# Kernel tuning notes

Measured on AMD Instinct MI355X. Metric: run time of the kernel, lower is better.

Reference implementation:

```python
import jax, jax.numpy as jnp
import numpy as np
import math


def _align_seq_len(e, target_n):
    # e: (B, H, N_enc, hd) -> (B, H, target_n, hd) via bilinear resize on sqrt grid
    B, H, N_enc, D = e.shape
    if N_enc == target_n:
        return e
    h_e = int(math.sqrt(N_enc))
    h_t = int(math.sqrt(target_n))
    img = jnp.transpose(e, (0, 1, 3, 2)).reshape(B, H, D, h_e, h_e)
    img = jax.image.resize(img, (B, H, D, h_t, h_t), method='bilinear')
    return jnp.transpose(img.reshape(B, H, D, target_n), (0, 1, 3, 2))


def setup_inputs() -> dict:
    key = jax.random.key(0)
    ks = jax.random.split(key, 7)
    B, N, D, H = 4, 1024, 1152, 16
    hd = D // H
    N_enc = 1024
    s_in = 1.0 / math.sqrt(D)
    return {
        'x': jax.random.normal(ks[0], (B, N, D), jnp.float32),
        'enc_k': jax.random.normal(ks[1], (B, H, N_enc, hd), jnp.float32),
        'enc_v': jax.random.normal(ks[2], (B, H, N_enc, hd), jnp.float32),
        'qkv_w': jax.random.normal(ks[3], (3 * D, D), jnp.float32) * s_in,
        'qkv_b': jax.random.normal(ks[4], (3 * D,), jnp.float32) * 0.02,
        'proj_w': jax.random.normal(ks[5], (D, D), jnp.float32) * s_in,
        'proj_b': jax.random.normal(ks[6], (D,), jnp.float32) * 0.02,
        'stage': 2,
    }


def reference(x, enc_k, enc_v, qkv_w, qkv_b, proj_w, proj_b, stage):
    B, N, C = x.shape
    H = enc_k.shape[1]
    hd = C // H
    scale = hd ** (-0.5)

    qkv = (x @ qkv_w.T + qkv_b).reshape(B, N, 3, H, hd)
    qkv = jnp.transpose(qkv, (2, 0, 3, 1, 4))  # (3, B, H, N, hd)
    q, k, v = qkv[0], qkv[1], qkv[2]

    distill_loss = jnp.float32(0.0)
    if stage == 1:
        ek = _align_seq_len(enc_k, N)
        ev = _align_seq_len(enc_v, N)
        attn = jax.nn.softmax(jnp.einsum('bhnd,bhmd->bhnm', q * scale, ek), axis=-1)
        x_out = jnp.einsum('bhnm,bhmd->bhnd', attn, ev)
    elif stage == 2:
        ek = _align_seq_len(enc_k, N)
        ev = _align_seq_len(enc_v, N)
        attn_own = jax.nn.softmax(jnp.einsum('bhnd,bhmd->bhnm', q * scale, k), axis=-1)
        x_out = jnp.einsum('bhnm,bhmd->bhnd', attn_own, v)
        qd = jax.lax.stop_gradient(q)
        attn_enc = jax.nn.softmax(jnp.einsum('bhnd,bhmd->bhnm', qd * scale, ek), axis=-1)
        o_star = jax.lax.stop_gradient(jnp.einsum('bhnm,bhmd->bhnd', attn_enc, ev))
        distill_loss = jnp.mean((x_out - o_star) ** 2)
    else:
        attn = jax.nn.softmax(jnp.einsum('bhnd,bhmd->bhnm', q * scale, k), axis=-1)
        x_out = jnp.einsum('bhnm,bhmd->bhnd', attn, v)

    x_out = jnp.transpose(x_out, (0, 2, 1, 3)).reshape(B, N, C)
    out = x_out @ proj_w.T + proj_b
    return out, distill_loss
```

## Files before the change

kernel.cpp:

```cpp
#include <hip/hip_runtime.h>
#include <hip/hip_bf16.h>

#define PB 4
#define PN 1024
#define PC 1152
#define PH 16
#define PHD 72
#define BH 64
#define QKV_COLS 3456
#define OUT_ELEMS ((size_t)PB*PN*PC)
#define K_DIM 1152

#define CHUNK_HALVES 6144
#define HEAD_HALVES (16*CHUNK_HALVES)
#define BUF_HALVES ((size_t)BH*HEAD_HALVES)

typedef _Float16 half8_t __attribute__((ext_vector_type(8)));
typedef _Float16 half4_t __attribute__((ext_vector_type(4)));
typedef float float4v __attribute__((ext_vector_type(4)));

#define QSCALE (0.11785113019775792f * 1.4426950408889634f)

__device__ __forceinline__ void load16_lds(const _Float16* g, _Float16* l) {
    __builtin_amdgcn_global_load_lds(
        (const __attribute__((address_space(1))) void*)g,
        (__attribute__((address_space(3))) void*)l, 16, 0, 0);
}

__global__ __launch_bounds__(256) void f32_to_f16(
    const float* __restrict__ in, _Float16* __restrict__ out, int n8)
{
    int i = blockIdx.x * 256 + threadIdx.x;
    if (i >= n8) return;
    float4 a = ((const float4*)in)[2 * i];
    float4 b = ((const float4*)in)[2 * i + 1];
    half8_t h;
    h[0] = (_Float16)a.x; h[1] = (_Float16)a.y; h[2] = (_Float16)a.z; h[3] = (_Float16)a.w;
    h[4] = (_Float16)b.x; h[5] = (_Float16)b.y; h[6] = (_Float16)b.z; h[7] = (_Float16)b.w;
    ((half8_t*)out)[i] = h;
}

__global__ __launch_bounds__(256) void zero_qpad(_Float16* __restrict__ qh)
{
    int i = blockIdx.x * 256 + threadIdx.x;
    int chunk = i / 192, within = i - chunk * 192;
    half8_t z = {};
    *(half8_t*)(qh + (size_t)chunk * CHUNK_HALVES + 4608 + within * 8) = z;
}

__global__ __launch_bounds__(256) void enc_convert(
    const float* __restrict__ ek, const float* __restrict__ ev,
    _Float16* __restrict__ ekh, _Float16* __restrict__ evth)
{
    const int bh = blockIdx.y, nblk = blockIdx.x, t = threadIdx.x;
    const float* ksrc = ek + ((size_t)bh * PN + nblk * 64) * PHD;
    const float* vsrc = ev + ((size_t)bh * PN + nblk * 64) * PHD;
    _Float16* kdst = ekh  + ((size_t)bh * 16 + nblk) * CHUNK_HALVES;
    _Float16* vdst = evth + ((size_t)bh * 16 + nblk) * CHUNK_HALVES;
    for (int i = t; i < 64 * 18; i += 256) {
        int n = i / 18, d4 = (i % 18) * 4;
        float4 kv = *(const float4*)&ksrc[n * PHD + d4];
        float4 vv = *(const float4*)&vsrc[n * PHD + d4];
        float ka[4] = {kv.x, kv.y, kv.z, kv.w};
        float va[4] = {vv.x, vv.y, vv.z, vv.w};
#pragma unroll
        for (int kk = 0; kk < 4; ++kk) {
            int d = d4 + kk;
            kdst[(d >> 3) * 512 + n * 8 + (d & 7)] = (_Float16)ka[kk];
            vdst[(n >> 3) * 768 + d * 8 + (n & 7)] = (_Float16)va[kk];
        }
    }
}

template<int MODE>
__global__ __launch_bounds__(256) void gemm_mfma(
    const _Float16* __restrict__ A, const _Float16* __restrict__ Bm,
    const float* __restrict__ bias,
    _Float16* __restrict__ qh, _Float16* __restrict__ kh,
    _Float16* __restrict__ vth, float* __restrict__ out, int c_tiles)
{
    const int t    = threadIdx.x;
    const int lane = t & 63;
    const int w    = t >> 6;
    const int wm   = w >> 1, wn = w & 1;
    const int lrow = lane & 15, quad = lane >> 4;

    const int per_group = c_tiles * 8;
    const int g  = blockIdx.x / per_group;
    const int r_ = blockIdx.x - g * per_group;
    const int m0 = (g * 8 + (r_ & 7)) * 128;
    const int c0 = (r_ >> 3) * 128;

    const bool tr = (MODE == 1) || (c0 < 2 * PC);

    __shared__ _Float16 As[8192];
    __shared__ _Float16 Bs[8192];

    int rowS[4], koff[4], ldsOff[4];
#pragma unroll
    for (int i = 0; i < 4; ++i) {
        int idx = w * 256 + i * 64 + lane;
        int kt2 = idx >> 9, qq = (idx >> 7) & 3;
        rowS[i]   = idx & 127;
        koff[i]   = kt2 * 32 + qq * 8;
        ldsOff[i] = idx * 8;
    }

    const _Float16* aBase = A  + (size_t)m0 * K_DIM;
    const _Float16* bBase = Bm + (size_t)c0 * K_DIM;

    float4v acc[4][4];
#pragma unroll
    for (int ti = 0; ti < 4; ++ti)
#pragma unroll
        for (int tj = 0; tj < 4; ++tj)
            acc[ti][tj] = (float4v){0.f, 0.f, 0.f, 0.f};

    for (int kb = 0; kb < K_DIM; kb += 64) {
        __syncthreads();
#pragma unroll
        for (int i = 0; i < 4; ++i) {
            load16_lds(aBase + (size_t)rowS[i] * K_DIM + kb + koff[i], &As[ldsOff[i]]);
            load16_lds(bBase + (size_t)rowS[i] * K_DIM + kb + koff[i], &Bs[ldsOff[i]]);
        }
        __syncthreads();
#pragma unroll
        for (int s = 0; s < 2; ++s) {
            half8_t af[4], bf[4];
#pragma unroll
            for (int ti = 0; ti < 4; ++ti)
                af[ti] = *(const half8_t*)&As[(((s * 4 + quad) * 128) + wm * 64 + ti * 16 + lrow) * 8];
#pragma unroll
            for (int tj = 0; tj < 4; ++tj)
                bf[tj] = *(const half8_t*)&Bs[(((s * 4 + quad) * 128) + wn * 64 + tj * 16 + lrow) * 8];
            if (tr) {
#pragma unroll
                for (int ti = 0; ti < 4; ++ti)
#pragma unroll
                    for (int tj = 0; tj < 4; ++tj)
                        acc[ti][tj] = __builtin_amdgcn_mfma_f32_16x16x32_f16(
                            bf[tj], af[ti], acc[ti][tj], 0, 0, 0);
            } else {
#pragma unroll
                for (int ti = 0; ti < 4; ++ti)
#pragma unroll
                    for (int tj = 0; tj < 4; ++tj)
                        acc[ti][tj] = __builtin_amdgcn_mfma_f32_16x16x32_f16(
                            af[ti], bf[tj], acc[ti][tj], 0, 0, 0);
            }
        }
    }

    if (MODE == 1) {
#pragma unroll
        for (int tj = 0; tj < 4; ++tj) {
            int cg = c0 + wn * 64 + tj * 16 + quad * 4;
            float4v bv = *(const float4v*)&bias[cg];
#pragma unroll
            for (int ti = 0; ti < 4; ++ti) {
                int m = m0 + wm * 64 + ti * 16 + lrow;
                float4v o;
#pragma unroll
                for (int r = 0; r < 4; ++r) o[r] = acc[ti][tj][r] + bv[r];
                *(float4v*)&out[(size_t)m * PC + cg] = o;
            }
        }
    } else if (tr) {
        const int jq = c0 / PC;
        const float mulv = (jq == 0) ? QSCALE : 1.f;
        _Float16* dstp = (jq == 0) ? qh : kh;
#pragma unroll
        for (int tj = 0; tj < 4; ++tj) {
            int cg  = c0 + wn * 64 + tj * 16 + quad * 4;
            int rem = cg - jq * PC;
            int h   = rem / PHD;
            int ds  = rem - h * PHD;
            float4v bv = *(const float4v*)&bias[cg];
#pragma unroll
            for (int ti = 0; ti < 4; ++ti) {
                int m = m0 + wm * 64 + ti * 16 + lrow;
                int b = m >> 10, n = m & 1023;
                size_t chunk = ((size_t)(b * PH + h) * 16 + (n >> 6)) * CHUNK_HALVES;
                half4_t hv;
#pragma unroll
                for (int r = 0; r < 4; ++r)
                    hv[r] = (_Float16)((acc[ti][tj][r] + bv[r]) * mulv);
                *(half4_t*)&dstp[chunk + (ds >> 3) * 512 + (n & 63) * 8 + (ds & 7)] = hv;
            }
        }
    } else {
#pragma unroll
        for (int tj = 0; tj < 4; ++tj) {
            int c   = c0 + wn * 64 + tj * 16 + lrow;
            int rem = c - 2 * PC;
            int h   = rem / PHD;
            int d   = rem - h * PHD;
            float bv = bias[c];
#pragma unroll
            for (int ti = 0; ti < 4; ++ti) {
                int mg = m0 + wm * 64 + ti * 16 + quad * 4;
                int b = mg >> 10, n = mg & 1023;
                size_t chunk = ((size_t)(b * PH + h) * 16 + (n >> 6)) * CHUNK_HALVES;
                half4_t hv;
#pragma unroll
                for (int r = 0; r < 4; ++r)
                    hv[r] = (_Float16)(acc[ti][tj][r] + bv);
                *(half4_t*)&vth[chunk + ((n & 63) >> 3) * 768 + d * 8 + (n & 7)] = hv;
            }
        }
    }
}

__device__ __forceinline__ void attn_step(
    const half8_t* qf, const _Float16* Ks, const _Float16* Vts, _Float16* Pw,
    float4v* O, float& m_run, float& l_run, int ln, int quad)
{
    float4v accS[4];
#pragma unroll
    for (int ct = 0; ct < 4; ++ct) accS[ct] = (float4v){0.f, 0.f, 0.f, 0.f};
#pragma unroll
    for (int ks = 0; ks < 3; ++ks) {
#pragma unroll
        for (int ct = 0; ct < 4; ++ct) {
            half8_t kf = *(const half8_t*)&Ks[(((ks * 4 + quad) * 64) + ct * 16 + ln) * 8];
            accS[ct] = __builtin_amdgcn_mfma_f32_16x16x32_f16(kf, qf[ks], accS[ct], 0, 0, 0);
        }
    }

    float mx = -1e30f;
#pragma unroll
    for (int ct = 0; ct < 4; ++ct)
#pragma unroll
        for (int r = 0; r < 4; ++r) mx = fmaxf(mx, accS[ct][r]);
    mx = fmaxf(mx, __shfl_xor(mx, 16));
    mx = fmaxf(mx, __shfl_xor(mx, 32));
    float m_new = fmaxf(m_run, mx);
    float alpha = exp2f(m_run - m_new);
    m_run = m_new;

    float lsum = 0.f;
    const int pbase = (quad >> 1) * 128 + ln * 8 + (quad & 1) * 4;
#pragma unroll
    for (int ct = 0; ct < 4; ++ct) {
        half4_t pk;
#pragma unroll
        for (int r = 0; r < 4; ++r) {
            float p = exp2f(accS[ct][r] - m_new);
            lsum += p;
            pk[r] = (_Float16)p;
        }
        *(half4_t*)&Pw[pbase + ct * 256] = pk;
    }
    lsum += __shfl_xor(lsum, 16);
    lsum += __shfl_xor(lsum, 32);
    l_run = l_run * alpha + lsum;

#pragma unroll
    for (int ct = 0; ct < 5; ++ct) O[ct] *= alpha;

#pragma unroll
    for (int ks = 0; ks < 2; ++ks) {
        half8_t pf = *(const half8_t*)&Pw[(ks * 4 + quad) * 128 + ln * 8];
#pragma unroll
        for (int ct = 0; ct < 5; ++ct) {
            half8_t vf = *(const half8_t*)&Vts[(((ks * 4 + quad) * 96) + ct * 16 + ln) * 8];
            O[ct] = __builtin_amdgcn_mfma_f32_16x16x32_f16(vf, pf, O[ct], 0, 0, 0);
        }
    }
}

__global__ __launch_bounds__(256, 4) void attn_fused(
    const _Float16* __restrict__ qh, const _Float16* __restrict__ kh,
    const _Float16* __restrict__ vth,
    const _Float16* __restrict__ ekh, const _Float16* __restrict__ evth,
    _Float16* __restrict__ xouth, float* __restrict__ loss_out)
{
    const int t = threadIdx.x;
    const int lane = t & 63;
    const int w = t >> 6;
    const int ln = lane & 15;
    const int quad = lane >> 4;

    const int lid  = blockIdx.x;
    const int bh   = (lid & 7) * 8 + ((lid >> 3) >> 4);
    const int nblk = (lid >> 3) & 15;

    __shared__ _Float16 Ks[CHUNK_HALVES];
    __shared__ _Float16 Vs[CHUNK_HALVES];
    __shared__ _Float16 Ps[4096];
    __shared__ float red[256];

    _Float16* Pw = Ps + w * 1024;

    const _Float16* qc = qh + ((size_t)bh * 16 + nblk) * CHUNK_HALVES;
    half8_t qf[3];
#pragma unroll
    for (int ks = 0; ks < 3; ++ks)
        qf[ks] = *(const half8_t*)&qc[(((ks * 4 + quad) * 64) + w * 16 + ln) * 8];

    const _Float16* kbo = kh   + (size_t)bh * HEAD_HALVES;
    const _Float16* vbo = vth  + (size_t)bh * HEAD_HALVES;
    const _Float16* kbe = ekh  + (size_t)bh * HEAD_HALVES;
    const _Float16* vbe = evth + (size_t)bh * HEAD_HALVES;

    float4v Oo[5], Oe[5];
#pragma unroll
    for (int ct = 0; ct < 5; ++ct) {
        Oo[ct] = (float4v){0.f, 0.f, 0.f, 0.f};
        Oe[ct] = (float4v){0.f, 0.f, 0.f, 0.f};
    }
    float m_o = -1e30f, l_o = 0.f;
    float m_e = -1e30f, l_e = 0.f;

    for (int kt = 0; kt < 16; ++kt) {
        const _Float16* kc = kbo + (size_t)kt * CHUNK_HALVES;
        const _Float16* vc = vbo + (size_t)kt * CHUNK_HALVES;
        __syncthreads();
#pragma unroll
        for (int i = 0; i < 3; ++i) {
            int u = i * 256 + t;
            load16_lds(kc + u * 8, &Ks[u * 8]);
            load16_lds(vc + u * 8, &Vs[u * 8]);
        }
        __syncthreads();
        attn_step(qf, Ks, Vs, Pw, Oo, m_o, l_o, ln, quad);
    }
    for (int kt = 0; kt < 16; ++kt) {
        const _Float16* kc = kbe + (size_t)kt * CHUNK_HALVES;
        const _Float16* vc = vbe + (size_t)kt * CHUNK_HALVES;
        __syncthreads();
#pragma unroll
        for (int i = 0; i < 3; ++i) {
            int u = i * 256 + t;
            load16_lds(kc + u * 8, &Ks[u * 8]);
            load16_lds(vc + u * 8, &Vs[u * 8]);
        }
        __syncthreads();
        attn_step(qf, Ks, Vs, Pw, Oe, m_e, l_e, ln, quad);
    }

    const float inv_o = 1.0f / l_o;
    const float inv_e = 1.0f / l_e;

    const int b = bh >> 4, h = bh & 15;
    const int nrow = nblk * 64 + w * 16 + ln;

    float lacc = 0.f;
    const size_t rowbase = (size_t)(b * PN + nrow) * PC + h * PHD;
#pragma unroll
    for (int ct = 0; ct < 5; ++ct) {
        int d0 = ct * 16 + quad * 4;
        if (d0 < PHD) {
            half4_t oh;
#pragma unroll
            for (int r = 0; r < 4; ++r) {
                float own = Oo[ct][r] * inv_o;
                oh[r] = (_Float16)own;
                float df = own - Oe[ct][r] * inv_e;
                lacc += df * df;
            }
            *(half4_t*)&xouth[rowbase + d0] = oh;
        }
    }

    red[t] = lacc;
    __syncthreads();
    for (int off = 128; off > 0; off >>= 1) {
        if (t < off) red[t] += red[t + off];
        __syncthreads();
    }
    if (t == 0) atomicAdd(loss_out, red[0] * (1.0f / (float)OUT_ELEMS));
}

extern "C" void kernel_launch(void* const* d_in, const int* in_sizes, int n_in,
                              void* d_out, int out_size, void* d_ws, size_t ws_size,
                              hipStream_t stream)
{
    const float* x      = (const float*)d_in[0];
    const float* enc_k  = (const float*)d_in[1];
    const float* enc_v  = (const float*)d_in[2];
    const float* qkv_w  = (const float*)d_in[3];
    const float* qkv_b  = (const float*)d_in[4];
    const float* proj_w = (const float*)d_in[5];
    const float* proj_b = (const float*)d_in[6];

    float* out = (float*)d_out;

    _Float16* x_h     = (_Float16*)d_ws;
    _Float16* qkvw_h  = x_h + OUT_ELEMS;
    _Float16* projw_h = qkvw_h + (size_t)QKV_COLS * PC;
    _Float16* xout_h  = projw_h + (size_t)PC * PC;
    _Float16* q_h     = xout_h + OUT_ELEMS;
    _Float16* k_h     = q_h  + BUF_HALVES;
    _Float16* vt_h    = k_h  + BUF_HALVES;
    _Float16* ek_h    = vt_h + BUF_HALVES;
    _Float16* evt_h   = ek_h + BUF_HALVES;

    const int n8_x  = (int)(OUT_ELEMS / 8);
    const int n8_qw = QKV_COLS * PC / 8;
    const int n8_pw = PC * PC / 8;

    hipMemsetAsync(out + OUT_ELEMS, 0, sizeof(float), stream);
    zero_qpad<<<768, 256, 0, stream>>>(q_h);

    f32_to_f16<<<(n8_x  + 255) / 256, 256, 0, stream>>>(x,      x_h,     n8_x);
    f32_to_f16<<<(n8_qw + 255) / 256, 256, 0, stream>>>(qkv_w,  qkvw_h,  n8_qw);
    f32_to_f16<<<(n8_pw + 255) / 256, 256, 0, stream>>>(proj_w, projw_h, n8_pw);
    enc_convert<<<dim3(16, BH), 256, 0, stream>>>(enc_k, enc_v, ek_h, evt_h);

    gemm_mfma<0><<<(QKV_COLS / 128) * ((PB * PN) / 128), 256, 0, stream>>>(
        x_h, qkvw_h, qkv_b, q_h, k_h, vt_h, nullptr, QKV_COLS / 128);

    attn_fused<<<16 * BH, 256, 0, stream>>>(
        q_h, k_h, vt_h, ek_h, evt_h, xout_h, out + OUT_ELEMS);

    gemm_mfma<1><<<(PC / 128) * ((PB * PN) / 128), 256, 0, stream>>>(
        xout_h, projw_h, proj_b, nullptr, nullptr, nullptr, out, PC / 128);
}
```

Measured before the change: 342.8 us.

## Merge prep kernels and give each attention wave two query tiles

Five preprocessing launches (three fp32-to-fp16 conversions, Q-pad zeroing, encoder K/V conversion) become one kernel that dispatches on block index, removing launch overhead. The attention kernel now runs 128 threads per block, and each wave handles two 16-row query tiles, so every K/V fragment read from LDS feeds two MFMAs. This halves LDS reads per FLOP and allows more independent MFMAs in flight. The cost is more accumulator registers (four sets of O), fewer waves per block to hide latency, and the removed occupancy hint on launch bounds.

```diff
diff --git a/kernel.cpp b/kernel.cpp
--- a/kernel.cpp
+++ b/kernel.cpp
@@ -27,11 +27,9 @@
         (__attribute__((address_space(3))) void*)l, 16, 0, 0);
 }
 
-__global__ __launch_bounds__(256) void f32_to_f16(
-    const float* __restrict__ in, _Float16* __restrict__ out, int n8)
-{
-    int i = blockIdx.x * 256 + threadIdx.x;
-    if (i >= n8) return;
+__device__ __forceinline__ void cvt8(const float* __restrict__ in,
+                                     _Float16* __restrict__ out, int i)
+{
     float4 a = ((const float4*)in)[2 * i];
     float4 b = ((const float4*)in)[2 * i + 1];
     half8_t h;
@@ -40,34 +38,45 @@
     ((half8_t*)out)[i] = h;
 }
 
-__global__ __launch_bounds__(256) void zero_qpad(_Float16* __restrict__ qh)
-{
-    int i = blockIdx.x * 256 + threadIdx.x;
-    int chunk = i / 192, within = i - chunk * 192;
-    half8_t z = {};
-    *(half8_t*)(qh + (size_t)chunk * CHUNK_HALVES + 4608 + within * 8) = z;
-}
-
-__global__ __launch_bounds__(256) void enc_convert(
+__global__ __launch_bounds__(256) void prep(
+    const float* __restrict__ x, const float* __restrict__ qkv_w,
+    const float* __restrict__ proj_w,
     const float* __restrict__ ek, const float* __restrict__ ev,
+    _Float16* __restrict__ x_h, _Float16* __restrict__ qkvw_h,
+    _Float16* __restrict__ projw_h, _Float16* __restrict__ qh,
     _Float16* __restrict__ ekh, _Float16* __restrict__ evth)
 {
-    const int bh = blockIdx.y, nblk = blockIdx.x, t = threadIdx.x;
-    const float* ksrc = ek + ((size_t)bh * PN + nblk * 64) * PHD;
-    const float* vsrc = ev + ((size_t)bh * PN + nblk * 64) * PHD;
-    _Float16* kdst = ekh  + ((size_t)bh * 16 + nblk) * CHUNK_HALVES;
-    _Float16* vdst = evth + ((size_t)bh * 16 + nblk) * CHUNK_HALVES;
-    for (int i = t; i < 64 * 18; i += 256) {
-        int n = i / 18, d4 = (i % 18) * 4;
-        float4 kv = *(const float4*)&ksrc[n * PHD + d4];
-        float4 vv = *(const float4*)&vsrc[n * PHD + d4];
-        float ka[4] = {kv.x, kv.y, kv.z, kv.w};
-        float va[4] = {vv.x, vv.y, vv.z, vv.w};
-#pragma unroll
-        for (int kk = 0; kk < 4; ++kk) {
-            int d = d4 + kk;
-            kdst[(d >> 3) * 512 + n * 8 + (d & 7)] = (_Float16)ka[kk];
-            vdst[(n >> 3) * 768 + d * 8 + (n & 7)] = (_Float16)va[kk];
+    const int b = blockIdx.x, t = threadIdx.x;
+    if (b < 2304) {
+        cvt8(x, x_h, b * 256 + t);
+    } else if (b < 4248) {
+        cvt8(qkv_w, qkvw_h, (b - 2304) * 256 + t);
+    } else if (b < 4896) {
+        cvt8(proj_w, projw_h, (b - 4248) * 256 + t);
+    } else if (b < 5664) {
+        int i = (b - 4896) * 256 + t;
+        int chunk = i / 192, within = i - chunk * 192;
+        half8_t z = {};
+        *(half8_t*)(qh + (size_t)chunk * CHUNK_HALVES + 4608 + within * 8) = z;
+    } else {
+        int bid = b - 5664;
+        int bh = bid >> 4, nblk = bid & 15;
+        const float* ksrc = ek + ((size_t)bh * PN + nblk * 64) * PHD;
+        const float* vsrc = ev + ((size_t)bh * PN + nblk * 64) * PHD;
+        _Float16* kdst = ekh  + ((size_t)bh * 16 + nblk) * CHUNK_HALVES;
+        _Float16* vdst = evth + ((size_t)bh * 16 + nblk) * CHUNK_HALVES;
+        for (int i = t; i < 64 * 18; i += 256) {
+            int n = i / 18, d4 = (i % 18) * 4;
+            float4 kv = *(const float4*)&ksrc[n * PHD + d4];
+            float4 vv = *(const float4*)&vsrc[n * PHD + d4];
+            float ka[4] = {kv.x, kv.y, kv.z, kv.w};
+            float va[4] = {vv.x, vv.y, vv.z, vv.w};
+#pragma unroll
+            for (int kk = 0; kk < 4; ++kk) {
+                int d = d4 + kk;
+                kdst[(d >> 3) * 512 + n * 8 + (d & 7)] = (_Float16)ka[kk];
+                vdst[(n >> 3) * 768 + d * 8 + (n & 7)] = (_Float16)va[kk];
+            }
         }
     }
 }
@@ -211,65 +220,77 @@
     }
 }
 
-__device__ __forceinline__ void attn_step(
-    const half8_t* qf, const _Float16* Ks, const _Float16* Vts, _Float16* Pw,
-    float4v* O, float& m_run, float& l_run, int ln, int quad)
-{
-    float4v accS[4];
-#pragma unroll
-    for (int ct = 0; ct < 4; ++ct) accS[ct] = (float4v){0.f, 0.f, 0.f, 0.f};
+__device__ __forceinline__ void attn_step2(
+    const half8_t qf[2][3], const _Float16* Ks, const _Float16* Vts,
+    _Float16* P0, _Float16* P1,
+    float4v O0[5], float4v O1[5], float m_run[2], float l_run[2],
+    int ln, int quad)
+{
+    float4v accS[2][4];
+#pragma unroll
+    for (int s = 0; s < 2; ++s)
+#pragma unroll
+        for (int ct = 0; ct < 4; ++ct) accS[s][ct] = (float4v){0.f, 0.f, 0.f, 0.f};
 #pragma unroll
     for (int ks = 0; ks < 3; ++ks) {
 #pragma unroll
         for (int ct = 0; ct < 4; ++ct) {
             half8_t kf = *(const half8_t*)&Ks[(((ks * 4 + quad) * 64) + ct * 16 + ln) * 8];
-            accS[ct] = __builtin_amdgcn_mfma_f32_16x16x32_f16(kf, qf[ks], accS[ct], 0, 0, 0);
-        }
-    }
-
-    float mx = -1e30f;
-#pragma unroll
-    for (int ct = 0; ct < 4; ++ct)
-#pragma unroll
-        for (int r = 0; r < 4; ++r) mx = fmaxf(mx, accS[ct][r]);
-    mx = fmaxf(mx, __shfl_xor(mx, 16));
-    mx = fmaxf(mx, __shfl_xor(mx, 32));
-    float m_new = fmaxf(m_run, mx);
-    float alpha = exp2f(m_run - m_new);
-    m_run = m_new;
-
-    float lsum = 0.f;
+            accS[0][ct] = __builtin_amdgcn_mfma_f32_16x16x32_f16(kf, qf[0][ks], accS[0][ct], 0, 0, 0);
+            accS[1][ct] = __builtin_amdgcn_mfma_f32_16x16x32_f16(kf, qf[1][ks], accS[1][ct], 0, 0, 0);
+        }
+    }
+
     const int pbase = (quad >> 1) * 128 + ln * 8 + (quad & 1) * 4;
 #pragma unroll
-    for (int ct = 0; ct < 4; ++ct) {
-        half4_t pk;
-#pragma unroll
-        for (int r = 0; r < 4; ++r) {
-            float p = exp2f(accS[ct][r] - m_new);
-            lsum += p;
-            pk[r] = (_Float16)p;
-        }
-        *(half4_t*)&Pw[pbase + ct * 256] = pk;
-    }
-    lsum += __shfl_xor(lsum, 16);
-    lsum += __shfl_xor(lsum, 32);
-    l_run = l_run * alpha + lsum;
-
-#pragma unroll
-    for (int ct = 0; ct < 5; ++ct) O[ct] *= alpha;
+    for (int s = 0; s < 2; ++s) {
+        _Float16* Pr = s ? P1 : P0;
+        float mx = -1e30f;
+#pragma unroll
+        for (int ct = 0; ct < 4; ++ct)
+#pragma unroll
+            for (int r = 0; r < 4; ++r) mx = fmaxf(mx, accS[s][ct][r]);
+        mx = fmaxf(mx, __shfl_xor(mx, 16));
+        mx = fmaxf(mx, __shfl_xor(mx, 32));
+        float m_new = fmaxf(m_run[s], mx);
+        float alpha = exp2f(m_run[s] - m_new);
+        m_run[s] = m_new;
+
+        float lsum = 0.f;
+#pragma unroll
+        for (int ct = 0; ct < 4; ++ct) {
+            half4_t pk;
+#pragma unroll
+            for (int r = 0; r < 4; ++r) {
+                float p = exp2f(accS[s][ct][r] - m_new);
+                lsum += p;
+                pk[r] = (_Float16)p;
+            }
+            *(half4_t*)&Pr[pbase + ct * 256] = pk;
+        }
+        lsum += __shfl_xor(lsum, 16);
+        lsum += __shfl_xor(lsum, 32);
+        l_run[s] = l_run[s] * alpha + lsum;
+
+        float4v* O = s ? O1 : O0;
+#pragma unroll
+        for (int ct = 0; ct < 5; ++ct) O[ct] *= alpha;
+    }
 
 #pragma unroll
     for (int ks = 0; ks < 2; ++ks) {
-        half8_t pf = *(const half8_t*)&Pw[(ks * 4 + quad) * 128 + ln * 8];
+        half8_t pf0 = *(const half8_t*)&P0[(ks * 4 + quad) * 128 + ln * 8];
+        half8_t pf1 = *(const half8_t*)&P1[(ks * 4 + quad) * 128 + ln * 8];
 #pragma unroll
         for (int ct = 0; ct < 5; ++ct) {
             half8_t vf = *(const half8_t*)&Vts[(((ks * 4 + quad) * 96) + ct * 16 + ln) * 8];
-            O[ct] = __builtin_amdgcn_mfma_f32_16x16x32_f16(vf, pf, O[ct], 0, 0, 0);
-        }
-    }
-}
-
-__global__ __launch_bounds__(256, 4) void attn_fused(
+            O0[ct] = __builtin_amdgcn_mfma_f32_16x16x32_f16(vf, pf0, O0[ct], 0, 0, 0);
+            O1[ct] = __builtin_amdgcn_mfma_f32_16x16x32_f16(vf, pf1, O1[ct], 0, 0, 0);
+        }
+    }
+}
+
+__global__ __launch_bounds__(128) void attn_fused(
     const _Float16* __restrict__ qh, const _Float16* __restrict__ kh,
     const _Float16* __restrict__ vth,
     const _Float16* __restrict__ ekh, const _Float16* __restrict__ evth,
@@ -288,84 +309,92 @@
     __shared__ _Float16 Ks[CHUNK_HALVES];
     __shared__ _Float16 Vs[CHUNK_HALVES];
     __shared__ _Float16 Ps[4096];
-    __shared__ float red[256];
-
-    _Float16* Pw = Ps + w * 1024;
+    __shared__ float red[128];
+
+    _Float16* P0 = Ps + w * 2048;
+    _Float16* P1 = P0 + 1024;
 
     const _Float16* qc = qh + ((size_t)bh * 16 + nblk) * CHUNK_HALVES;
-    half8_t qf[3];
-#pragma unroll
-    for (int ks = 0; ks < 3; ++ks)
-        qf[ks] = *(const half8_t*)&qc[(((ks * 4 + quad) * 64) + w * 16 + ln) * 8];
+    half8_t qf[2][3];
+#pragma unroll
+    for (int s = 0; s < 2; ++s)
+#pragma unroll
+        for (int ks = 0; ks < 3; ++ks)
+            qf[s][ks] = *(const half8_t*)&qc[(((ks * 4 + quad) * 64) + w * 32 + s * 16 + ln) * 8];
 
     const _Float16* kbo = kh   + (size_t)bh * HEAD_HALVES;
     const _Float16* vbo = vth  + (size_t)bh * HEAD_HALVES;
     const _Float16* kbe = ekh  + (size_t)bh * HEAD_HALVES;
     const _Float16* vbe = evth + (size_t)bh * HEAD_HALVES;
 
-    float4v Oo[5], Oe[5];
+    float4v Oo0[5], Oo1[5], Oe0[5], Oe1[5];
 #pragma unroll
     for (int ct = 0; ct < 5; ++ct) {
-        Oo[ct] = (float4v){0.f, 0.f, 0.f, 0.f};
-        Oe[ct] = (float4v){0.f, 0.f, 0.f, 0.f};
-    }
-    float m_o = -1e30f, l_o = 0.f;
-    float m_e = -1e30f, l_e = 0.f;
+        Oo0[ct] = (float4v){0.f, 0.f, 0.f, 0.f};
+        Oo1[ct] = (float4v){0.f, 0.f, 0.f, 0.f};
+        Oe0[ct] = (float4v){0.f, 0.f, 0.f, 0.f};
+        Oe1[ct] = (float4v){0.f, 0.f, 0.f, 0.f};
+    }
+    float m_o[2] = {-1e30f, -1e30f}, l_o[2] = {0.f, 0.f};
+    float m_e[2] = {-1e30f, -1e30f}, l_e[2] = {0.f, 0.f};
 
     for (int kt = 0; kt < 16; ++kt) {
         const _Float16* kc = kbo + (size_t)kt * CHUNK_HALVES;
         const _Float16* vc = vbo + (size_t)kt * CHUNK_HALVES;
         __syncthreads();
 #pragma unroll
-        for (int i = 0; i < 3; ++i) {
-            int u = i * 256 + t;
+        for (int i = 0; i < 6; ++i) {
+            int u = i * 128 + t;
             load16_lds(kc + u * 8, &Ks[u * 8]);
             load16_lds(vc + u * 8, &Vs[u * 8]);
         }
         __syncthreads();
-        attn_step(qf, Ks, Vs, Pw, Oo, m_o, l_o, ln, quad);
+        attn_step2(qf, Ks, Vs, P0, P1, Oo0, Oo1, m_o, l_o, ln, quad);
     }
     for (int kt = 0; kt < 16; ++kt) {
         const _Float16* kc = kbe + (size_t)kt * CHUNK_HALVES;
         const _Float16* vc = vbe + (size_t)kt * CHUNK_HALVES;
         __syncthreads();
 #pragma unroll
-        for (int i = 0; i < 3; ++i) {
-            int u = i * 256 + t;
+        for (int i = 0; i < 6; ++i) {
+            int u = i * 128 + t;
             load16_lds(kc + u * 8, &Ks[u * 8]);
             load16_lds(vc + u * 8, &Vs[u * 8]);
         }
         __syncthreads();
-        attn_step(qf, Ks, Vs, Pw, Oe, m_e, l_e, ln, quad);
-    }
-
-    const float inv_o = 1.0f / l_o;
-    const float inv_e = 1.0f / l_e;
+        attn_step2(qf, Ks, Vs, P0, P1, Oe0, Oe1, m_e, l_e, ln, quad);
+    }
 
     const int b = bh >> 4, h = bh & 15;
-    const int nrow = nblk * 64 + w * 16 + ln;
-
     float lacc = 0.f;
-    const size_t rowbase = (size_t)(b * PN + nrow) * PC + h * PHD;
-#pragma unroll
-    for (int ct = 0; ct < 5; ++ct) {
-        int d0 = ct * 16 + quad * 4;
-        if (d0 < PHD) {
-            half4_t oh;
-#pragma unroll
-            for (int r = 0; r < 4; ++r) {
-                float own = Oo[ct][r] * inv_o;
-                oh[r] = (_Float16)own;
-                float df = own - Oe[ct][r] * inv_e;
-                lacc += df * df;
-            }
-            *(half4_t*)&xouth[rowbase + d0] = oh;
+#pragma unroll
+    for (int s = 0; s < 2; ++s) {
+        const float4v* Oo = s ? Oo1 : Oo0;
+        const float4v* Oe = s ? Oe1 : Oe0;
+        const float inv_o = 1.0f / l_o[s];
+        const float inv_e = 1.0f / l_e[s];
+        const int nrow = nblk * 64 + w * 32 + s * 16 + ln;
+        const size_t rowbase = (size_t)(b * PN + nrow) * PC + h * PHD;
+#pragma unroll
+        for (int ct = 0; ct < 5; ++ct) {
+            int d0 = ct * 16 + quad * 4;
+            if (d0 < PHD) {
+                half4_t oh;
+#pragma unroll
+                for (int r = 0; r < 4; ++r) {
+                    float own = Oo[ct][r] * inv_o;
+                    oh[r] = (_Float16)own;
+                    float df = own - Oe[ct][r] * inv_e;
+                    lacc += df * df;
+                }
+                *(half4_t*)&xouth[rowbase + d0] = oh;
+            }
         }
     }
 
     red[t] = lacc;
     __syncthreads();
-    for (int off = 128; off > 0; off >>= 1) {
+    for (int off = 64; off > 0; off >>= 1) {
         if (t < off) red[t] += red[t + off];
         __syncthreads();
     }
@@ -396,22 +425,15 @@
     _Float16* ek_h    = vt_h + BUF_HALVES;
     _Float16* evt_h   = ek_h + BUF_HALVES;
 
-    const int n8_x  = (int)(OUT_ELEMS / 8);
-    const int n8_qw = QKV_COLS * PC / 8;
-    const int n8_pw = PC * PC / 8;
-
     hipMemsetAsync(out + OUT_ELEMS, 0, sizeof(float), stream);
-    zero_qpad<<<768, 256, 0, stream>>>(q_h);
-
-    f32_to_f16<<<(n8_x  + 255) / 256, 256, 0, stream>>>(x,      x_h,     n8_x);
-    f32_to_f16<<<(n8_qw + 255) / 256, 256, 0, stream>>>(qkv_w,  qkvw_h,  n8_qw);
-    f32_to_f16<<<(n8_pw + 255) / 256, 256, 0, stream>>>(proj_w, projw_h, n8_pw);
-    enc_convert<<<dim3(16, BH), 256, 0, stream>>>(enc_k, enc_v, ek_h, evt_h);
+
+    prep<<<6688, 256, 0, stream>>>(x, qkv_w, proj_w, enc_k, enc_v,
+                                   x_h, qkvw_h, projw_h, q_h, ek_h, evt_h);
 
     gemm_mfma<0><<<(QKV_COLS / 128) * ((PB * PN) / 128), 256, 0, stream>>>(
         x_h, qkvw_h, qkv_b, q_h, k_h, vt_h, nullptr, QKV_COLS / 128);
 
-    attn_fused<<<16 * BH, 256, 0, stream>>>(
+    attn_fused<<<16 * BH, 128, 0, stream>>>(
         q_h, k_h, vt_h, ek_h, evt_h, xout_h, out + OUT_ELEMS);
 
     gemm_mfma<1><<<(PC / 128) * ((PB * PN) / 128), 256, 0, stream>>>(
```

Result: slower. 426.9 us (+24.5%).

## Double-buffer 32-key attention sub-tiles and merge prep kernels into one launch

Applied to the files above, without the earlier changes.

The attention loop now works on 32-key sub-tiles. Their K and V are staged into double-buffered LDS, so the next sub-tile's global-to-LDS load overlaps the current sub-tile's MFMA work, and each iteration has one barrier instead of two. The K layouts in the QKV GEMM epilogue and the encoder conversion change to match the 32-row sub-chunks. The four conversion and zeroing kernels are merged into a single prep launch to cut launch overhead. The cost is twice as many loop iterations with smaller MFMA batches and more softmax rescales, and the `__launch_bounds__` occupancy hint of 4 is dropped.

```diff
diff --git a/kernel.cpp b/kernel.cpp
--- a/kernel.cpp
+++ b/kernel.cpp
@@ -12,6 +12,7 @@
 #define K_DIM 1152
 
 #define CHUNK_HALVES 6144
+#define SUB_HALVES 3072
 #define HEAD_HALVES (16*CHUNK_HALVES)
 #define BUF_HALVES ((size_t)BH*HEAD_HALVES)
 
@@ -27,11 +28,9 @@
         (__attribute__((address_space(3))) void*)l, 16, 0, 0);
 }
 
-__global__ __launch_bounds__(256) void f32_to_f16(
-    const float* __restrict__ in, _Float16* __restrict__ out, int n8)
-{
-    int i = blockIdx.x * 256 + threadIdx.x;
-    if (i >= n8) return;
+__device__ __forceinline__ void cvt8(const float* __restrict__ in,
+                                     _Float16* __restrict__ out, int i)
+{
     float4 a = ((const float4*)in)[2 * i];
     float4 b = ((const float4*)in)[2 * i + 1];
     half8_t h;
@@ -40,34 +39,45 @@
     ((half8_t*)out)[i] = h;
 }
 
-__global__ __launch_bounds__(256) void zero_qpad(_Float16* __restrict__ qh)
-{
-    int i = blockIdx.x * 256 + threadIdx.x;
-    int chunk = i / 192, within = i - chunk * 192;
-    half8_t z = {};
-    *(half8_t*)(qh + (size_t)chunk * CHUNK_HALVES + 4608 + within * 8) = z;
-}
-
-__global__ __launch_bounds__(256) void enc_convert(
+__global__ __launch_bounds__(256) void prep(
+    const float* __restrict__ x, const float* __restrict__ qkv_w,
+    const float* __restrict__ proj_w,
     const float* __restrict__ ek, const float* __restrict__ ev,
+    _Float16* __restrict__ x_h, _Float16* __restrict__ qkvw_h,
+    _Float16* __restrict__ projw_h, _Float16* __restrict__ qh,
     _Float16* __restrict__ ekh, _Float16* __restrict__ evth)
 {
-    const int bh = blockIdx.y, nblk = blockIdx.x, t = threadIdx.x;
-    const float* ksrc = ek + ((size_t)bh * PN + nblk * 64) * PHD;
-    const float* vsrc = ev + ((size_t)bh * PN + nblk * 64) * PHD;
-    _Float16* kdst = ekh  + ((size_t)bh * 16 + nblk) * CHUNK_HALVES;
-    _Float16* vdst = evth + ((size_t)bh * 16 + nblk) * CHUNK_HALVES;
-    for (int i = t; i < 64 * 18; i += 256) {
-        int n = i / 18, d4 = (i % 18) * 4;
-        float4 kv = *(const float4*)&ksrc[n * PHD + d4];
-        float4 vv = *(const float4*)&vsrc[n * PHD + d4];
-        float ka[4] = {kv.x, kv.y, kv.z, kv.w};
-        float va[4] = {vv.x, vv.y, vv.z, vv.w};
-#pragma unroll
-        for (int kk = 0; kk < 4; ++kk) {
-            int d = d4 + kk;
-            kdst[(d >> 3) * 512 + n * 8 + (d & 7)] = (_Float16)ka[kk];
-            vdst[(n >> 3) * 768 + d * 8 + (n & 7)] = (_Float16)va[kk];
+    const int b = blockIdx.x, t = threadIdx.x;
+    if (b < 2304) {
+        cvt8(x, x_h, b * 256 + t);
+    } else if (b < 4248) {
+        cvt8(qkv_w, qkvw_h, (b - 2304) * 256 + t);
+    } else if (b < 4896) {
+        cvt8(proj_w, projw_h, (b - 4248) * 256 + t);
+    } else if (b < 5664) {
+        int i = (b - 4896) * 256 + t;
+        int chunk = i / 192, within = i - chunk * 192;
+        half8_t z = {};
+        *(half8_t*)(qh + (size_t)chunk * CHUNK_HALVES + 4608 + within * 8) = z;
+    } else {
+        int bid = b - 5664;
+        int bh = bid >> 4, nblk = bid & 15;
+        const float* ksrc = ek + ((size_t)bh * PN + nblk * 64) * PHD;
+        const float* vsrc = ev + ((size_t)bh * PN + nblk * 64) * PHD;
+        _Float16* kdst = ekh  + ((size_t)bh * 16 + nblk) * CHUNK_HALVES;
+        _Float16* vdst = evth + ((size_t)bh * 16 + nblk) * CHUNK_HALVES;
+        for (int i = t; i < 64 * 18; i += 256) {
+            int n = i / 18, d4 = (i % 18) * 4;
+            float4 kv = *(const float4*)&ksrc[n * PHD + d4];
+            float4 vv = *(const float4*)&vsrc[n * PHD + d4];
+            float ka[4] = {kv.x, kv.y, kv.z, kv.w};
+            float va[4] = {vv.x, vv.y, vv.z, vv.w};
+#pragma unroll
+            for (int kk = 0; kk < 4; ++kk) {
+                int d = d4 + kk;
+                kdst[(n >> 5) * SUB_HALVES + (d >> 3) * 256 + (n & 31) * 8 + (d & 7)] = (_Float16)ka[kk];
+                vdst[(n >> 3) * 768 + d * 8 + (n & 7)] = (_Float16)va[kk];
+            }
         }
     }
 }
@@ -185,7 +195,11 @@
 #pragma unroll
                 for (int r = 0; r < 4; ++r)
                     hv[r] = (_Float16)((acc[ti][tj][r] + bv[r]) * mulv);
-                *(half4_t*)&dstp[chunk + (ds >> 3) * 512 + (n & 63) * 8 + (ds & 7)] = hv;
+                if (jq == 0)
+                    *(half4_t*)&dstp[chunk + (ds >> 3) * 512 + (n & 63) * 8 + (ds & 7)] = hv;
+                else
+                    *(half4_t*)&dstp[chunk + ((n & 63) >> 5) * SUB_HALVES
+                                     + (ds >> 3) * 256 + (n & 31) * 8 + (ds & 7)] = hv;
             }
         }
     } else {
@@ -211,27 +225,37 @@
     }
 }
 
-__device__ __forceinline__ void attn_step(
-    const half8_t* qf, const _Float16* Ks, const _Float16* Vts, _Float16* Pw,
-    float4v* O, float& m_run, float& l_run, int ln, int quad)
-{
-    float4v accS[4];
-#pragma unroll
-    for (int ct = 0; ct < 4; ++ct) accS[ct] = (float4v){0.f, 0.f, 0.f, 0.f};
+__device__ __forceinline__ void stage_sub(
+    const _Float16* kc, const _Float16* vc,
+    _Float16* Ks, _Float16* Vs, int w, int lane)
+{
+#pragma unroll
+    for (int i = 0; i < 3; ++i) {
+        int seg = i * 4 + w;
+        const _Float16* src = (seg < 6) ? kc + seg * 512 : vc + (seg - 6) * 512;
+        _Float16*       dst = (seg < 6) ? Ks + seg * 512 : Vs + (seg - 6) * 512;
+        load16_lds(src + lane * 8, dst + lane * 8);
+    }
+}
+
+__device__ __forceinline__ void attn_sub(
+    const half8_t qf[3], const _Float16* Ks, const _Float16* Vs, _Float16* Pw,
+    float4v O[5], float& m_run, float& l_run, int ln, int quad)
+{
+    float4v accS[2];
+#pragma unroll
+    for (int ct = 0; ct < 2; ++ct) accS[ct] = (float4v){0.f, 0.f, 0.f, 0.f};
 #pragma unroll
     for (int ks = 0; ks < 3; ++ks) {
 #pragma unroll
-        for (int ct = 0; ct < 4; ++ct) {
-            half8_t kf = *(const half8_t*)&Ks[(((ks * 4 + quad) * 64) + ct * 16 + ln) * 8];
+        for (int ct = 0; ct < 2; ++ct) {
+            half8_t kf = *(const half8_t*)&Ks[(((ks * 4 + quad) * 32) + ct * 16 + ln) * 8];
             accS[ct] = __builtin_amdgcn_mfma_f32_16x16x32_f16(kf, qf[ks], accS[ct], 0, 0, 0);
         }
     }
 
-    float mx = -1e30f;
-#pragma unroll
-    for (int ct = 0; ct < 4; ++ct)
-#pragma unroll
-        for (int r = 0; r < 4; ++r) mx = fmaxf(mx, accS[ct][r]);
+    float mx = fmaxf(fmaxf(fmaxf(accS[0][0], accS[0][1]), fmaxf(accS[0][2], accS[0][3])),
+                     fmaxf(fmaxf(accS[1][0], accS[1][1]), fmaxf(accS[1][2], accS[1][3])));
     mx = fmaxf(mx, __shfl_xor(mx, 16));
     mx = fmaxf(mx, __shfl_xor(mx, 32));
     float m_new = fmaxf(m_run, mx);
@@ -241,7 +265,7 @@
     float lsum = 0.f;
     const int pbase = (quad >> 1) * 128 + ln * 8 + (quad & 1) * 4;
 #pragma unroll
-    for (int ct = 0; ct < 4; ++ct) {
+    for (int ct = 0; ct < 2; ++ct) {
         half4_t pk;
 #pragma unroll
         for (int r = 0; r < 4; ++r) {
@@ -258,18 +282,15 @@
 #pragma unroll
     for (int ct = 0; ct < 5; ++ct) O[ct] *= alpha;
 
-#pragma unroll
-    for (int ks = 0; ks < 2; ++ks) {
-        half8_t pf = *(const half8_t*)&Pw[(ks * 4 + quad) * 128 + ln * 8];
-#pragma unroll
-        for (int ct = 0; ct < 5; ++ct) {
-            half8_t vf = *(const half8_t*)&Vts[(((ks * 4 + quad) * 96) + ct * 16 + ln) * 8];
-            O[ct] = __builtin_amdgcn_mfma_f32_16x16x32_f16(vf, pf, O[ct], 0, 0, 0);
-        }
-    }
-}
-
-__global__ __launch_bounds__(256, 4) void attn_fused(
+    half8_t pf = *(const half8_t*)&Pw[quad * 128 + ln * 8];
+#pragma unroll
+    for (int ct = 0; ct < 5; ++ct) {
+        half8_t vf = *(const half8_t*)&Vs[(quad * 96 + ct * 16 + ln) * 8];
+        O[ct] = __builtin_amdgcn_mfma_f32_16x16x32_f16(vf, pf, O[ct], 0, 0, 0);
+    }
+}
+
+__global__ __launch_bounds__(256) void attn_fused(
     const _Float16* __restrict__ qh, const _Float16* __restrict__ kh,
     const _Float16* __restrict__ vth,
     const _Float16* __restrict__ ekh, const _Float16* __restrict__ evth,
@@ -285,12 +306,12 @@
     const int bh   = (lid & 7) * 8 + ((lid >> 3) >> 4);
     const int nblk = (lid >> 3) & 15;
 
-    __shared__ _Float16 Ks[CHUNK_HALVES];
-    __shared__ _Float16 Vs[CHUNK_HALVES];
-    __shared__ _Float16 Ps[4096];
+    __shared__ _Float16 Ks[2][SUB_HALVES];
+    __shared__ _Float16 Vs[2][SUB_HALVES];
+    __shared__ _Float16 Ps[2048];
     __shared__ float red[256];
 
-    _Float16* Pw = Ps + w * 1024;
+    _Float16* Pw = Ps + w * 512;
 
     const _Float16* qc = qh + ((size_t)bh * 16 + nblk) * CHUNK_HALVES;
     half8_t qf[3];
@@ -312,31 +333,26 @@
     float m_o = -1e30f, l_o = 0.f;
     float m_e = -1e30f, l_e = 0.f;
 
-    for (int kt = 0; kt < 16; ++kt) {
-        const _Float16* kc = kbo + (size_t)kt * CHUNK_HALVES;
-        const _Float16* vc = vbo + (size_t)kt * CHUNK_HALVES;
+    stage_sub(kbo, vbo, Ks[0], Vs[0], w, lane);
+    __syncthreads();
+
+    for (int s = 0; s < 32; ++s) {
+        const int cur = s & 1, nxt = cur ^ 1;
+        if (s < 31)
+            stage_sub(kbo + (s + 1) * SUB_HALVES, vbo + (s + 1) * SUB_HALVES,
+                      Ks[nxt], Vs[nxt], w, lane);
+        else
+            stage_sub(kbe, vbe, Ks[nxt], Vs[nxt], w, lane);
+        attn_sub(qf, Ks[cur], Vs[cur], Pw, Oo, m_o, l_o, ln, quad);
         __syncthreads();
-#pragma unroll
-        for (int i = 0; i < 3; ++i) {
-            int u = i * 256 + t;
-            load16_lds(kc + u * 8, &Ks[u * 8]);
-            load16_lds(vc + u * 8, &Vs[u * 8]);
-        }
+    }
+    for (int s = 0; s < 32; ++s) {
+        const int cur = s & 1, nxt = cur ^ 1;
+        if (s < 31)
+            stage_sub(kbe + (s + 1) * SUB_HALVES, vbe + (s + 1) * SUB_HALVES,
+                      Ks[nxt], Vs[nxt], w, lane);
+        attn_sub(qf, Ks[cur], Vs[cur], Pw, Oe, m_e, l_e, ln, quad);
         __syncthreads();
-        attn_step(qf, Ks, Vs, Pw, Oo, m_o, l_o, ln, quad);
-    }
-    for (int kt = 0; kt < 16; ++kt) {
-        const _Float16* kc = kbe + (size_t)kt * CHUNK_HALVES;
-        const _Float16* vc = vbe + (size_t)kt * CHUNK_HALVES;
-        __syncthreads();
-#pragma unroll
-        for (int i = 0; i < 3; ++i) {
-            int u = i * 256 + t;
-            load16_lds(kc + u * 8, &Ks[u * 8]);
-            load16_lds(vc + u * 8, &Vs[u * 8]);
-        }
-        __syncthreads();
-        attn_step(qf, Ks, Vs, Pw, Oe, m_e, l_e, ln, quad);
     }
 
     const float inv_o = 1.0f / l_o;
@@ -396,17 +412,10 @@
     _Float16* ek_h    = vt_h + BUF_HALVES;
     _Float16* evt_h   = ek_h + BUF_HALVES;
 
-    const int n8_x  = (int)(OUT_ELEMS / 8);
-    const int n8_qw = QKV_COLS * PC / 8;
-    const int n8_pw = PC * PC / 8;
-
     hipMemsetAsync(out + OUT_ELEMS, 0, sizeof(float), stream);
-    zero_qpad<<<768, 256, 0, stream>>>(q_h);
-
-    f32_to_f16<<<(n8_x  + 255) / 256, 256, 0, stream>>>(x,      x_h,     n8_x);
-    f32_to_f16<<<(n8_qw + 255) / 256, 256, 0, stream>>>(qkv_w,  qkvw_h,  n8_qw);
-    f32_to_f16<<<(n8_pw + 255) / 256, 256, 0, stream>>>(proj_w, projw_h, n8_pw);
-    enc_convert<<<dim3(16, BH), 256, 0, stream>>>(enc_k, enc_v, ek_h, evt_h);
+
+    prep<<<6688, 256, 0, stream>>>(x, qkv_w, proj_w, enc_k, enc_v,
+                                   x_h, qkvw_h, projw_h, q_h, ek_h, evt_h);
 
     gemm_mfma<0><<<(QKV_COLS / 128) * ((PB * PN) / 128), 256, 0, stream>>>(
         x_h, qkvw_h, qkv_b, q_h, k_h, vt_h, nullptr, QKV_COLS / 128);
```

Result: slower. 375.4 us (+9.5%).
